# Performance work log

Measured on AMD Instinct MI355X. Metric: run time of the kernel, lower is better.

## Reference

```python
import jax, jax.numpy as jnp
import numpy as np
import math

B, S, DK, DV = 8, 2048, 128, 128
SQRT_DK = math.sqrt(DK)


def setup_inputs() -> dict:
    key = jax.random.key(0)
    kq, kk, kv = jax.random.split(key, 3)
    Q = jax.random.normal(kq, (B, S, DK), dtype=jnp.float32)
    K = jax.random.normal(kk, (B, S, DK), dtype=jnp.float32)
    V = jax.random.normal(kv, (B, S, DV), dtype=jnp.float32)
    # additive causal mask, broadcast over batch: 0 on/below diag, -1e9 above
    causal = jnp.tril(jnp.ones((S, S), dtype=bool))
    mask = jnp.where(causal, 0.0, -1e9).astype(jnp.float32)[None]  # [1, S, S]
    return {"Q": Q, "K": K, "V": V, "mask": mask}


def reference(Q, K, V, mask):
    # QK = Q @ K^T / sqrt(dk); dropout is identity in eval mode.
    scores = jnp.einsum("bqd,bkd->bqk", Q, K) / SQRT_DK + mask  # [B, S, S]
    # transpose->softmax(dim=1)->transpose == softmax over key axis (last dim)
    A = jax.nn.softmax(scores, axis=-1)
    return jnp.einsum("bqk,bkv->bqv", A, V)  # [B, S, DV]
```

## Files before the change

### kernel.cpp

```cpp
#include <hip/hip_runtime.h>

#define SEQ 2048
#define DHEAD 128
#define NB 8
#define PSTRIDE 72
#define KSTRIDE 136
#define VSTRIDE 72

typedef short short8 __attribute__((ext_vector_type(8)));
typedef float f32x4 __attribute__((ext_vector_type(4)));

__device__ __forceinline__ unsigned short f2bf(float x) {
    unsigned int u = __float_as_uint(x);
    u += 0x7fffu + ((u >> 16) & 1u);
    return (unsigned short)(u >> 16);
}

__global__ void convert_bf16(const float* __restrict__ src, unsigned short* __restrict__ dst,
                             int n4) {
    int i = blockIdx.x * blockDim.x + threadIdx.x;
    if (i < n4) {
        float4 v = ((const float4*)src)[i];
        ushort4 o;
        o.x = f2bf(v.x); o.y = f2bf(v.y); o.z = f2bf(v.z); o.w = f2bf(v.w);
        ((ushort4*)dst)[i] = o;
    }
}

__global__ void transpose_v(const float* __restrict__ V, unsigned short* __restrict__ Vt) {
    __shared__ unsigned short t[32][33];
    int b = blockIdx.y;
    int s0 = (blockIdx.x >> 2) << 5;
    int d0 = (blockIdx.x & 3) << 5;
    int tid = threadIdx.x;
    int sl = tid >> 3, dl = (tid & 7) << 2;
    float4 v = *(const float4*)&V[(b * SEQ + s0 + sl) * DHEAD + d0 + dl];
    t[sl][dl + 0] = f2bf(v.x); t[sl][dl + 1] = f2bf(v.y);
    t[sl][dl + 2] = f2bf(v.z); t[sl][dl + 3] = f2bf(v.w);
    __syncthreads();
    int dr = tid >> 3, sr = (tid & 7) << 2;
    ushort4 o;
    o.x = t[sr + 0][dr]; o.y = t[sr + 1][dr]; o.z = t[sr + 2][dr]; o.w = t[sr + 3][dr];
    *(ushort4*)&Vt[(b * DHEAD + d0 + dr) * SEQ + s0 + sr] = o;
}

__global__ __launch_bounds__(256, 3)
void flash_attn(const float* __restrict__ Q, const unsigned short* __restrict__ Kb,
                const unsigned short* __restrict__ Vt,
                float* __restrict__ Opart, float* __restrict__ lsumP) {
    __shared__ __align__(16) unsigned short Klds[64 * KSTRIDE];
    __shared__ __align__(16) unsigned short Vlds[128 * VSTRIDE];
    __shared__ __align__(16) unsigned short Pb[4][16 * PSTRIDE];

    const int b = blockIdx.x & 7;
    const int u = blockIdx.x >> 3;
    int qt, c;
    if (u < 8)       { qt = u;                c = 0; }
    else if (u < 24) { qt = 8 + ((u - 8) >> 1);   c = (u - 8) & 1; }
    else if (u < 48) { qt = 16 + (u - 24) / 3;    c = (u - 24) % 3; }
    else             { qt = 24 + ((u - 48) >> 2); c = (u - 48) & 3; }
    const int kt0 = c * 8;
    const int kt1 = min(qt + 1, kt0 + 8);

    const int tid = threadIdx.x;
    const int w = tid >> 6, lane = tid & 63;
    const int ln15 = lane & 15, g = lane >> 4;
    const int qrow0 = qt * 64 + w * 16;

    const float scale = 0.08838834764831845f;
    short8 qf[4];
    {
        const float* qp = Q + (b * SEQ + qrow0 + ln15) * DHEAD + g * 8;
#pragma unroll
        for (int cc = 0; cc < 4; ++cc) {
            float4 a = *(const float4*)(qp + cc * 32);
            float4 d = *(const float4*)(qp + cc * 32 + 4);
            short8 f;
            f[0] = f2bf(a.x * scale); f[1] = f2bf(a.y * scale);
            f[2] = f2bf(a.z * scale); f[3] = f2bf(a.w * scale);
            f[4] = f2bf(d.x * scale); f[5] = f2bf(d.y * scale);
            f[6] = f2bf(d.z * scale); f[7] = f2bf(d.w * scale);
            qf[cc] = f;
        }
    }

    f32x4 acc[8];
#pragma unroll
    for (int i = 0; i < 8; ++i) acc[i] = (f32x4){0.f, 0.f, 0.f, 0.f};
    float lsum[4] = {0.f, 0.f, 0.f, 0.f};
    unsigned short* P = &Pb[w][0];

    short8 pre[8];
    {
        const int k0 = kt0 << 6;
#pragma unroll
        for (int j = 0; j < 4; ++j) {
            int ck = tid + j * 256;
            pre[j]     = *(const short8*)(Kb + (b * SEQ + k0 + (ck >> 4)) * DHEAD + (ck & 15) * 8);
            pre[4 + j] = *(const short8*)(Vt + (b * DHEAD + (ck >> 3)) * SEQ + k0 + (ck & 7) * 8);
        }
#pragma unroll
        for (int j = 0; j < 4; ++j) {
            int ck = tid + j * 256;
            *(short8*)&Klds[(ck >> 4) * KSTRIDE + (ck & 15) * 8] = pre[j];
            *(short8*)&Vlds[(ck >> 3) * VSTRIDE + (ck & 7) * 8]  = pre[4 + j];
        }
    }
    __syncthreads();

    for (int kt = kt0; kt < kt1; ++kt) {
        const int k0 = kt << 6;
        const bool have_next = (kt + 1 < kt1);
        short8 pre2[8];
        if (have_next) {
            const int kn = (kt + 1) << 6;
#pragma unroll
            for (int j = 0; j < 4; ++j) {
                int ck = tid + j * 256;
                pre2[j]     = *(const short8*)(Kb + (b * SEQ + kn + (ck >> 4)) * DHEAD + (ck & 15) * 8);
                pre2[4 + j] = *(const short8*)(Vt + (b * DHEAD + (ck >> 3)) * SEQ + kn + (ck & 7) * 8);
            }
        }

        const bool diag = (kt == qt);
#pragma unroll
        for (int nt = 0; nt < 4; ++nt) {
            f32x4 s = (f32x4){0.f, 0.f, 0.f, 0.f};
#pragma unroll
            for (int cc = 0; cc < 4; ++cc) {
                short8 kf = *(const short8*)&Klds[(nt * 16 + ln15) * KSTRIDE + cc * 32 + g * 8];
                s = __builtin_amdgcn_mfma_f32_16x16x32_bf16(qf[cc], kf, s, 0, 0, 0);
            }
            const int colg = k0 + nt * 16 + ln15;
#pragma unroll
            for (int r = 0; r < 4; ++r) {
                float p = __expf(s[r]);
                if (diag) {
                    int rowg = qrow0 + g * 4 + r;
                    p = (colg <= rowg) ? p : 0.f;
                }
                lsum[r] += p;
                P[(g * 4 + r) * PSTRIDE + nt * 16 + ln15] = f2bf(p);
            }
        }
#pragma unroll
        for (int c2 = 0; c2 < 2; ++c2) {
            short8 pf = *(const short8*)&P[ln15 * PSTRIDE + c2 * 32 + g * 8];
#pragma unroll
            for (int nt2 = 0; nt2 < 8; ++nt2) {
                short8 vf = *(const short8*)&Vlds[(nt2 * 16 + ln15) * VSTRIDE + c2 * 32 + g * 8];
                acc[nt2] = __builtin_amdgcn_mfma_f32_16x16x32_bf16(pf, vf, acc[nt2], 0, 0, 0);
            }
        }

        if (have_next) {
            __syncthreads();
#pragma unroll
            for (int j = 0; j < 4; ++j) {
                int ck = tid + j * 256;
                *(short8*)&Klds[(ck >> 4) * KSTRIDE + (ck & 15) * 8] = pre2[j];
                *(short8*)&Vlds[(ck >> 3) * VSTRIDE + (ck & 7) * 8]  = pre2[4 + j];
            }
            __syncthreads();
        }
    }

#pragma unroll
    for (int r = 0; r < 4; ++r) {
        float v = lsum[r];
        v += __shfl_xor(v, 1);
        v += __shfl_xor(v, 2);
        v += __shfl_xor(v, 4);
        v += __shfl_xor(v, 8);
        lsum[r] = v;
    }
    if (ln15 == 0) {
#pragma unroll
        for (int r = 0; r < 4; ++r)
            lsumP[(c * NB + b) * SEQ + qrow0 + g * 4 + r] = lsum[r];
    }
#pragma unroll
    for (int nt2 = 0; nt2 < 8; ++nt2) {
#pragma unroll
        for (int r = 0; r < 4; ++r) {
            Opart[((c * NB + b) * SEQ + qrow0 + g * 4 + r) * DHEAD + nt2 * 16 + ln15] = acc[nt2][r];
        }
    }
}

__global__ void finalize(const float* __restrict__ Opart, const float* __restrict__ lsumP,
                         float* __restrict__ out) {
    int gid = blockIdx.x * blockDim.x + threadIdx.x;
    int d4 = gid & 31;
    int row = (gid >> 5) & 2047;
    int b = gid >> 16;
    int nch = (row >> 9) + 1;
    float4 o = {0.f, 0.f, 0.f, 0.f};
    float l = 0.f;
    for (int c = 0; c < nch; ++c) {
        float4 p = ((const float4*)Opart)[((c * NB + b) * SEQ + row) * 32 + d4];
        o.x += p.x; o.y += p.y; o.z += p.z; o.w += p.w;
        l += lsumP[(c * NB + b) * SEQ + row];
    }
    float inv = 1.0f / l;
    float4 r;
    r.x = o.x * inv; r.y = o.y * inv; r.z = o.z * inv; r.w = o.w * inv;
    ((float4*)out)[gid] = r;
}

extern "C" void kernel_launch(void* const* d_in, const int* in_sizes, int n_in,
                              void* d_out, int out_size, void* d_ws, size_t ws_size,
                              hipStream_t stream) {
    const float* Q = (const float*)d_in[0];
    const float* K = (const float*)d_in[1];
    const float* V = (const float*)d_in[2];
    float* out = (float*)d_out;

    const int NE = NB * SEQ * DHEAD;
    unsigned short* Kb = (unsigned short*)d_ws;
    unsigned short* Vt = Kb + NE;
    float* Opart = (float*)(Vt + NE);
    float* lsumP = Opart + 4 * NE;

    convert_bf16<<<NE / 4 / 256, 256, 0, stream>>>(K, Kb, NE / 4);
    transpose_v<<<dim3(256, NB), 256, 0, stream>>>(V, Vt);
    flash_attn<<<640, 256, 0, stream>>>(Q, Kb, Vt, Opart, lsumP);
    finalize<<<NB * SEQ * 32 / 256, 256, 0, stream>>>(Opart, lsumP, out);
}
```

Measured before the change: 116.0 us.

## Merge prep kernels, reorder work units longest-first, write single-chunk rows directly

Combines the K conversion and V transpose into one prep launch, removing one kernel launch. A constant table now orders the flash-attention work units so the longest chunks (those with the most key tiles) are dispatched first, which should improve load balance across CUs. Query tiles that need only one chunk (qt<8) normalize and write their output directly, so finalize skips the first 512 rows and less partial data goes through global memory. The cost is a table lookup per block and extra branching in the epilogue.

```diff
diff --git a/kernel.cpp b/kernel.cpp
--- a/kernel.cpp
+++ b/kernel.cpp
@@ -10,55 +10,64 @@
 typedef short short8 __attribute__((ext_vector_type(8)));
 typedef float f32x4 __attribute__((ext_vector_type(4)));
 
+__device__ __constant__ unsigned char UNIT[80] = {
+    124,125,126,127, 120,121,122, 116,117,118, 112,113,114, 108,109,110,
+    104,105,106, 96,97,98, 100,101,102, 92,93,94, 88,89, 84,85, 80,81,
+    76,77, 72,73, 68,69, 64,65, 60,61, 56, 52, 48, 44, 40, 36, 32, 28,
+    123, 90, 57, 24,
+    119, 86, 53, 20,
+    115, 82, 49, 16,
+    111, 78, 45, 12,
+    107, 74, 41,  8,
+    103, 70, 37,  4,
+     99, 66, 33,  0
+};
+
 __device__ __forceinline__ unsigned short f2bf(float x) {
     unsigned int u = __float_as_uint(x);
     u += 0x7fffu + ((u >> 16) & 1u);
     return (unsigned short)(u >> 16);
 }
 
-__global__ void convert_bf16(const float* __restrict__ src, unsigned short* __restrict__ dst,
-                             int n4) {
-    int i = blockIdx.x * blockDim.x + threadIdx.x;
-    if (i < n4) {
-        float4 v = ((const float4*)src)[i];
+__global__ void prep(const float* __restrict__ K, const float* __restrict__ V,
+                     unsigned short* __restrict__ Kb, unsigned short* __restrict__ Vt) {
+    if (blockIdx.x < 2048) {
+        int i = blockIdx.x * 256 + threadIdx.x;
+        float4 v = ((const float4*)K)[i];
         ushort4 o;
         o.x = f2bf(v.x); o.y = f2bf(v.y); o.z = f2bf(v.z); o.w = f2bf(v.w);
-        ((ushort4*)dst)[i] = o;
-    }
-}
-
-__global__ void transpose_v(const float* __restrict__ V, unsigned short* __restrict__ Vt) {
-    __shared__ unsigned short t[32][33];
-    int b = blockIdx.y;
-    int s0 = (blockIdx.x >> 2) << 5;
-    int d0 = (blockIdx.x & 3) << 5;
-    int tid = threadIdx.x;
-    int sl = tid >> 3, dl = (tid & 7) << 2;
-    float4 v = *(const float4*)&V[(b * SEQ + s0 + sl) * DHEAD + d0 + dl];
-    t[sl][dl + 0] = f2bf(v.x); t[sl][dl + 1] = f2bf(v.y);
-    t[sl][dl + 2] = f2bf(v.z); t[sl][dl + 3] = f2bf(v.w);
-    __syncthreads();
-    int dr = tid >> 3, sr = (tid & 7) << 2;
-    ushort4 o;
-    o.x = t[sr + 0][dr]; o.y = t[sr + 1][dr]; o.z = t[sr + 2][dr]; o.w = t[sr + 3][dr];
-    *(ushort4*)&Vt[(b * DHEAD + d0 + dr) * SEQ + s0 + sr] = o;
+        ((ushort4*)Kb)[i] = o;
+    } else {
+        __shared__ unsigned short t[32][33];
+        int bx = blockIdx.x - 2048;
+        int b = bx >> 8, xy = bx & 255;
+        int s0 = (xy >> 2) << 5;
+        int d0 = (xy & 3) << 5;
+        int tid = threadIdx.x;
+        int sl = tid >> 3, dl = (tid & 7) << 2;
+        float4 v = *(const float4*)&V[(b * SEQ + s0 + sl) * DHEAD + d0 + dl];
+        t[sl][dl + 0] = f2bf(v.x); t[sl][dl + 1] = f2bf(v.y);
+        t[sl][dl + 2] = f2bf(v.z); t[sl][dl + 3] = f2bf(v.w);
+        __syncthreads();
+        int dr = tid >> 3, sr = (tid & 7) << 2;
+        ushort4 o;
+        o.x = t[sr + 0][dr]; o.y = t[sr + 1][dr]; o.z = t[sr + 2][dr]; o.w = t[sr + 3][dr];
+        *(ushort4*)&Vt[(b * DHEAD + d0 + dr) * SEQ + s0 + sr] = o;
+    }
 }
 
 __global__ __launch_bounds__(256, 3)
 void flash_attn(const float* __restrict__ Q, const unsigned short* __restrict__ Kb,
                 const unsigned short* __restrict__ Vt,
-                float* __restrict__ Opart, float* __restrict__ lsumP) {
+                float* __restrict__ Opart, float* __restrict__ lsumP,
+                float* __restrict__ out) {
     __shared__ __align__(16) unsigned short Klds[64 * KSTRIDE];
     __shared__ __align__(16) unsigned short Vlds[128 * VSTRIDE];
     __shared__ __align__(16) unsigned short Pb[4][16 * PSTRIDE];
 
     const int b = blockIdx.x & 7;
-    const int u = blockIdx.x >> 3;
-    int qt, c;
-    if (u < 8)       { qt = u;                c = 0; }
-    else if (u < 24) { qt = 8 + ((u - 8) >> 1);   c = (u - 8) & 1; }
-    else if (u < 48) { qt = 16 + (u - 24) / 3;    c = (u - 24) % 3; }
-    else             { qt = 24 + ((u - 48) >> 2); c = (u - 48) & 3; }
+    const int e = UNIT[blockIdx.x >> 3];
+    const int qt = e >> 2, c = e & 3;
     const int kt0 = c * 8;
     const int kt1 = min(qt + 1, kt0 + 8);
 
@@ -90,9 +99,9 @@
     float lsum[4] = {0.f, 0.f, 0.f, 0.f};
     unsigned short* P = &Pb[w][0];
 
-    short8 pre[8];
     {
         const int k0 = kt0 << 6;
+        short8 pre[8];
 #pragma unroll
         for (int j = 0; j < 4; ++j) {
             int ck = tid + j * 256;
@@ -174,26 +183,38 @@
         v += __shfl_xor(v, 8);
         lsum[r] = v;
     }
-    if (ln15 == 0) {
-#pragma unroll
-        for (int r = 0; r < 4; ++r)
-            lsumP[(c * NB + b) * SEQ + qrow0 + g * 4 + r] = lsum[r];
-    }
-#pragma unroll
-    for (int nt2 = 0; nt2 < 8; ++nt2) {
-#pragma unroll
-        for (int r = 0; r < 4; ++r) {
-            Opart[((c * NB + b) * SEQ + qrow0 + g * 4 + r) * DHEAD + nt2 * 16 + ln15] = acc[nt2][r];
+
+    if (qt < 8) {
+#pragma unroll
+        for (int nt2 = 0; nt2 < 8; ++nt2) {
+#pragma unroll
+            for (int r = 0; r < 4; ++r) {
+                int rowg = qrow0 + g * 4 + r;
+                out[(b * SEQ + rowg) * DHEAD + nt2 * 16 + ln15] = acc[nt2][r] / lsum[r];
+            }
+        }
+    } else {
+        if (ln15 == 0) {
+#pragma unroll
+            for (int r = 0; r < 4; ++r)
+                lsumP[(c * NB + b) * SEQ + qrow0 + g * 4 + r] = lsum[r];
+        }
+#pragma unroll
+        for (int nt2 = 0; nt2 < 8; ++nt2) {
+#pragma unroll
+            for (int r = 0; r < 4; ++r) {
+                Opart[((c * NB + b) * SEQ + qrow0 + g * 4 + r) * DHEAD + nt2 * 16 + ln15] = acc[nt2][r];
+            }
         }
     }
 }
 
 __global__ void finalize(const float* __restrict__ Opart, const float* __restrict__ lsumP,
                          float* __restrict__ out) {
-    int gid = blockIdx.x * blockDim.x + threadIdx.x;
-    int d4 = gid & 31;
-    int row = (gid >> 5) & 2047;
-    int b = gid >> 16;
+    int b = blockIdx.y;
+    int gx = blockIdx.x * 256 + threadIdx.x;
+    int d4 = gx & 31;
+    int row = 512 + (gx >> 5);
     int nch = (row >> 9) + 1;
     float4 o = {0.f, 0.f, 0.f, 0.f};
     float l = 0.f;
@@ -205,7 +226,7 @@
     float inv = 1.0f / l;
     float4 r;
     r.x = o.x * inv; r.y = o.y * inv; r.z = o.z * inv; r.w = o.w * inv;
-    ((float4*)out)[gid] = r;
+    ((float4*)out)[(b * SEQ + row) * 32 + d4] = r;
 }
 
 extern "C" void kernel_launch(void* const* d_in, const int* in_sizes, int n_in,
@@ -222,8 +243,7 @@
     float* Opart = (float*)(Vt + NE);
     float* lsumP = Opart + 4 * NE;
 
-    convert_bf16<<<NE / 4 / 256, 256, 0, stream>>>(K, Kb, NE / 4);
-    transpose_v<<<dim3(256, NB), 256, 0, stream>>>(V, Vt);
-    flash_attn<<<640, 256, 0, stream>>>(Q, Kb, Vt, Opart, lsumP);
-    finalize<<<NB * SEQ * 32 / 256, 256, 0, stream>>>(Opart, lsumP, out);
-}
+    prep<<<4096, 256, 0, stream>>>(K, V, Kb, Vt);
+    flash_attn<<<640, 256, 0, stream>>>(Q, Kb, Vt, Opart, lsumP, out);
+    finalize<<<dim3(192, NB), 256, 0, stream>>>(Opart, lsumP, out);
+}
```

Result: faster. 113.1 us (-2.5%).
